# Kernel optimization log

Hardware: AMD Instinct MI355X
Metric: run time of the kernel (lower is better)

## Reference

```python
import jax, jax.numpy as jnp
import numpy as np

D_IN = 1024
D_OUT = 1024
NUM_HEADS = 16
HEAD_DIM = D_OUT // NUM_HEADS


def setup_inputs() -> dict:
    key = jax.random.key(0)
    ks = jax.random.split(key, 6)
    s = 1.0 / np.sqrt(D_IN)
    inputs = jax.random.normal(ks[0], (4, 2048, D_IN), dtype=jnp.float32)
    Wq = jax.random.uniform(ks[1], (D_IN, D_OUT), jnp.float32, -s, s)
    Wk = jax.random.uniform(ks[2], (D_IN, D_OUT), jnp.float32, -s, s)
    Wv = jax.random.uniform(ks[3], (D_IN, D_OUT), jnp.float32, -s, s)
    so = 1.0 / np.sqrt(D_OUT)
    Wo = jax.random.uniform(ks[4], (D_OUT, D_OUT), jnp.float32, -so, so)
    bo = jax.random.uniform(ks[5], (D_OUT,), jnp.float32, -so, so)
    return {"inputs": inputs, "Wq": Wq, "Wk": Wk, "Wv": Wv, "Wo": Wo, "bo": bo}


def reference(inputs, Wq, Wk, Wv, Wo, bo):
    b, n, _ = inputs.shape
    # projections -> [b, h, n, d]
    def split_heads(x):
        return x.reshape(b, n, NUM_HEADS, HEAD_DIM).transpose(0, 2, 1, 3)
    q = split_heads(inputs @ Wq)
    k = split_heads(inputs @ Wk)
    v = split_heads(inputs @ Wv)
    scores = jnp.einsum('bhqd,bhkd->bhqk', q, k) / np.sqrt(HEAD_DIM).astype(np.float32)
    causal = jnp.tril(jnp.ones((n, n), dtype=bool))  # True = keep
    scores = jnp.where(causal, scores, -jnp.inf)
    weights = jax.nn.softmax(scores, axis=-1)
    ctx = jnp.einsum('bhqk,bhkd->bhqd', weights, v)
    ctx = ctx.transpose(0, 2, 1, 3).reshape(b, n, D_OUT)
    return ctx @ Wo + bo
```

## Files before the change

kernel.cpp:

```cpp
#include <hip/hip_runtime.h>

typedef unsigned short u16;
typedef unsigned int u32;
typedef __attribute__((ext_vector_type(8))) short short8;
typedef __attribute__((ext_vector_type(4))) short short4_t;
typedef __attribute__((ext_vector_type(4))) float floatx4;
typedef __attribute__((ext_vector_type(4))) unsigned short ushort4_t;
typedef __attribute__((ext_vector_type(4))) float float4_t;
typedef __attribute__((ext_vector_type(2))) unsigned int uint2_t;


__device__ __forceinline__ u16 f2bf(float f) {
  unsigned u = __builtin_bit_cast(unsigned, f);
  u += 0x7FFFu + ((u >> 16) & 1u);
  return (u16)(u >> 16);
}

__device__ __forceinline__ u32 pack_bf2(float a, float b) {
  u32 ua = __builtin_bit_cast(u32, a) + 0x8000u;
  u32 ub = __builtin_bit_cast(u32, b) + 0x8000u;
  return __builtin_amdgcn_perm(ua, ub, 0x07060302u);
}

__device__ __forceinline__ void gload_lds16(const void* g, void* l) {
  __builtin_amdgcn_global_load_lds(
      (const __attribute__((address_space(1))) void*)g,
      (__attribute__((address_space(3))) void*)l, 16, 0, 0);
}

#define BAR __builtin_amdgcn_s_barrier()
#define LGK0                                              \
  do {                                                    \
    asm volatile("s_waitcnt lgkmcnt(0)" ::: "memory");    \
    __builtin_amdgcn_sched_barrier(0);                    \
  } while (0)
#define VM4 asm volatile("s_waitcnt vmcnt(4)" ::: "memory")
#define VM0 asm volatile("s_waitcnt vmcnt(0)" ::: "memory")


__global__ void cvt_x(const float* __restrict__ src, u16* __restrict__ dst) {
  int i = blockIdx.x * 256 + threadIdx.x;
  float4_t f = ((const float4_t*)src)[i];
  ushort4_t u;
  u.x = f2bf(f.x); u.y = f2bf(f.y); u.z = f2bf(f.z); u.w = f2bf(f.w);
  ((ushort4_t*)dst)[i] = u;
}

__global__ __launch_bounds__(256) void transpose_cvt4(
    const float* __restrict__ wq, const float* __restrict__ wk,
    const float* __restrict__ wv, const float* __restrict__ wo,
    u16* __restrict__ qk, u16* __restrict__ vt, u16* __restrict__ ot, float sc) {
  __shared__ float T[64][65];
  const int which = blockIdx.z;
  const float* s = (which == 0) ? wq : (which == 1) ? wk : (which == 2) ? wv : wo;
  u16* d = (which == 0) ? qk : (which == 1) ? (qk + (1u << 20)) : (which == 2) ? vt : ot;
  const float scale = (which == 0) ? sc : 1.f;
  const int n0 = blockIdx.x * 64, k0 = blockIdx.y * 64;
  const int c = threadIdx.x & 63, rg = threadIdx.x >> 6;
  for (int i = 0; i < 16; ++i) {
    int r = i * 4 + rg;
    T[r][c] = s[(k0 + r) * 1024 + n0 + c];
  }
  __syncthreads();
  for (int i = 0; i < 16; ++i) {
    int r = i * 4 + rg;
    d[(n0 + r) * 1024 + k0 + c] = f2bf(T[c][r] * scale);
  }
}

template <int MODE>
__global__ __launch_bounds__(256) void gemm_bt(
    const u16* __restrict__ A, const u16* __restrict__ Bt, void* __restrict__ Cv,
    const float* __restrict__ bias, int K, int lda, int ldb, int ldc) {
  __shared__ u16 As[2][128 * 32];
  __shared__ u16 Bs[2][128 * 32];
  const int tid = threadIdx.x;
  const int w = tid >> 6, l = tid & 63, quad = l >> 4, l16 = l & 15;
  const int wm = w >> 1, wn = w & 1;
  const size_t m0 = (size_t)blockIdx.y * 128, n0 = (size_t)blockIdx.x * 128;

  floatx4 acc[4][4];
  for (int i = 0; i < 4; ++i)
    for (int j = 0; j < 4; ++j) acc[i][j] = (floatx4){0.f, 0.f, 0.f, 0.f};

  auto stage = [&](int k0, int buf) {
    for (int i = 0; i < 2; ++i) {
      int c = i * 256 + tid;
      int row = c >> 2, off = (c & 3) * 8;
      gload_lds16(A + (m0 + row) * (size_t)lda + k0 + off, &As[buf][c * 8]);
      gload_lds16(Bt + (n0 + row) * (size_t)ldb + k0 + off, &Bs[buf][c * 8]);
    }
  };

  const int nk = K >> 5;
  stage(0, 0);
  __syncthreads();

  for (int ki = 0; ki < nk; ++ki) {
    const int buf = ki & 1;
    if (ki + 1 < nk) stage((ki + 1) << 5, buf ^ 1);

    short8 a[4], bb[4];
    for (int im = 0; im < 4; ++im)
      a[im] = *(const short8*)&As[buf][(wm * 64 + im * 16 + l16) * 32 + quad * 8];
    for (int in = 0; in < 4; ++in)
      bb[in] = *(const short8*)&Bs[buf][(wn * 64 + in * 16 + l16) * 32 + quad * 8];
    for (int im = 0; im < 4; ++im)
      for (int in = 0; in < 4; ++in)
        acc[im][in] = __builtin_amdgcn_mfma_f32_16x16x32_bf16(a[im], bb[in], acc[im][in], 0, 0, 0);

    __syncthreads();
  }

  for (int im = 0; im < 4; ++im)
    for (int in = 0; in < 4; ++in) {
      size_t r0 = m0 + wm * 64 + im * 16 + quad * 4;
      size_t col = n0 + wn * 64 + in * 16 + l16;
      float bv = (MODE == 1) ? bias[col] : 0.f;
      for (int r = 0; r < 4; ++r) {
        float val = acc[im][in][r] + bv;
        if (MODE == 0)
          ((u16*)Cv)[(r0 + r) * (size_t)ldc + col] = f2bf(val);
        else
          ((float*)Cv)[(r0 + r) * (size_t)ldc + col] = val;
      }
    }
}

__global__ __launch_bounds__(512, 2) void gemm256_bt(
    const u16* __restrict__ A, const u16* __restrict__ Bt, u16* __restrict__ C,
    int K, int lda, int ldb, int ldc) {
  __shared__ u16 As[2][256 * 64];
  __shared__ u16 Bs[2][256 * 64];
  const int tid = threadIdx.x;
  const int l = tid & 63, quad = l >> 4, l16 = l & 15;
  const int w = tid >> 6, wm = w >> 2, wn = w & 3;

  const int orig = blockIdx.x + 8 * blockIdx.y;
  const int tsw = (orig & 7) * 32 + (orig >> 3);
  const size_t m0 = (size_t)(tsw >> 3) * 256, n0 = (size_t)(tsw & 7) * 256;
  const int NT = K >> 6;

  floatx4 acc[8][4];
#pragma unroll
  for (int i = 0; i < 8; ++i)
#pragma unroll
    for (int j = 0; j < 4; ++j) acc[i][j] = (floatx4){0.f, 0.f, 0.f, 0.f};

  auto stage = [&](int isB, int t, int h) {
    const u16* src = isB ? Bt : A;
    const size_t rb = isB ? n0 : m0;
    const int ld = isB ? ldb : lda;
    u16* lds = (isB ? &Bs[t & 1][0] : &As[t & 1][0]) + h * 8192;
    const int k0 = t << 6;
#pragma unroll
    for (int r = 0; r < 2; ++r) {
      int idx = r * 512 + tid;
      int rr = idx >> 3;
      int ce = ((idx & 7) ^ (rr & 7)) << 3;
      gload_lds16(src + (rb + h * 128 + rr) * (size_t)ld + k0 + ce, lds + idx * 8);
    }
  };

  const int swz = (l16 & 7) << 4;
  const int ca0 = (quad * 16) ^ swz;
  const int ca1 = (64 + quad * 16) ^ swz;
  const char* aB = (const char*)&As[0][0];
  const char* bB = (const char*)&Bs[0][0];
  const int arow = (wm * 128 + l16) * 128;
  const int brow = (wn * 64 + l16) * 128;

  short8 a[4][2], b[2][2][2];

  auto readA = [&](int buf, int mh) {
#pragma unroll
    for (int ii = 0; ii < 4; ++ii) {
      const char* p = aB + buf * 32768 + arow + mh * 8192 + ii * 2048;
      a[ii][0] = *(const short8*)(p + ca0);
      a[ii][1] = *(const short8*)(p + ca1);
    }
  };
  auto readB = [&](int buf, int nh) {
#pragma unroll
    for (int jj = 0; jj < 2; ++jj) {
      const char* p = bB + buf * 32768 + brow + nh * 4096 + jj * 2048;
      b[nh][jj][0] = *(const short8*)(p + ca0);
      b[nh][jj][1] = *(const short8*)(p + ca1);
    }
  };
  auto mmaq = [&](int mh, int nh) {
    __builtin_amdgcn_s_setprio(1);
#pragma unroll
    for (int ii = 0; ii < 4; ++ii)
#pragma unroll
      for (int jj = 0; jj < 2; ++jj) {
        acc[mh * 4 + ii][nh * 2 + jj] = __builtin_amdgcn_mfma_f32_16x16x32_bf16(
            a[ii][0], b[nh][jj][0], acc[mh * 4 + ii][nh * 2 + jj], 0, 0, 0);
        acc[mh * 4 + ii][nh * 2 + jj] = __builtin_amdgcn_mfma_f32_16x16x32_bf16(
            a[ii][1], b[nh][jj][1], acc[mh * 4 + ii][nh * 2 + jj], 0, 0, 0);
      }
    __builtin_amdgcn_s_setprio(0);
  };

  stage(1, 0, 0); stage(1, 0, 1); stage(0, 0, 0); stage(0, 0, 1);
  stage(1, 1, 0); stage(1, 1, 1);
  VM4;
  BAR;

  const int nit = NT >> 1;
  for (int i = 0; i < nit; ++i) {
    const int t0 = 2 * i;
    const bool last = (i + 1 == nit);
    readA(0, 0); readB(0, 0);
    stage(0, t0 + 1, 0);
    BAR; LGK0; mmaq(0, 0); BAR;
    readB(0, 1);
    stage(0, t0 + 1, 1);
    BAR; LGK0; mmaq(0, 1); BAR;
    readA(0, 1);
    if (t0 + 2 < NT) stage(1, t0 + 2, 0);
    BAR; LGK0; mmaq(1, 1); BAR;
    if (t0 + 2 < NT) stage(1, t0 + 2, 1);
    mmaq(1, 0);
    if (last) { VM0; } else { VM4; }
    BAR;
    readA(1, 0); readB(1, 0);
    if (t0 + 2 < NT) stage(0, t0 + 2, 0);
    BAR; LGK0; mmaq(0, 0); BAR;
    readB(1, 1);
    if (t0 + 2 < NT) stage(0, t0 + 2, 1);
    BAR; LGK0; mmaq(0, 1); BAR;
    readA(1, 1);
    if (t0 + 3 < NT) stage(1, t0 + 3, 0);
    BAR; LGK0; mmaq(1, 1); BAR;
    if (t0 + 3 < NT) stage(1, t0 + 3, 1);
    mmaq(1, 0);
    VM4; BAR;
  }

#pragma unroll
  for (int iF = 0; iF < 8; ++iF)
#pragma unroll
    for (int jF = 0; jF < 4; ++jF) {
      size_t r0 = m0 + wm * 128 + iF * 16 + quad * 4;
      size_t col = n0 + wn * 64 + jF * 16 + l16;
#pragma unroll
      for (int r = 0; r < 4; ++r)
        C[(r0 + r) * (size_t)ldc + col] = f2bf(acc[iF][jF][r]);
    }
}

__global__ __launch_bounds__(256, 2) void flash_attn(
    const u16* __restrict__ QK, const u16* __restrict__ Vt, u16* __restrict__ ctx) {
  __shared__ u16 Ks[2][64 * 64];
  __shared__ u16 Vs[2][64 * 64];

  const int tid = threadIdx.x;
  const int w = tid >> 6, l = tid & 63, quad = l >> 4, l16 = l & 15;
  const int bh = blockIdx.x, p = blockIdx.y;
  const int b = bh >> 4, h = bh & 15;
  const int xr = (l16 & 7) << 4;

  const int qtA = 15 - p, qtB = p;
  const int nktA = 2 * qtA + 2, ntot = nktA + 2 * qtB + 2;

  auto stage = [&](int kt, int buf) {
    for (int i = 0; i < 2; ++i) {
      int c = i * 256 + tid;
      int row = c >> 3, scol = ((c & 7) ^ (row & 7)) << 3;
      gload_lds16(QK + (size_t)(b * 2048 + kt * 64 + row) * 2048 + 1024 + h * 64 + scol,
                  &Ks[buf][c * 8]);
      gload_lds16(Vt + (size_t)(h * 64 + row) * 8192 + b * 2048 + kt * 64 + scol,
                  &Vs[buf][c * 8]);
    }
  };

  short8 aq[2][2];
  floatx4 o[2][4];
  float lsum[2];

  auto load_q = [&](int q0w) {
    for (int qf = 0; qf < 2; ++qf) {
      const size_t base = (size_t)(b * 2048 + q0w + qf * 16 + l16) * 2048 + h * 64 + quad * 8;
      aq[qf][0] = *(const short8*)(QK + base);
      aq[qf][1] = *(const short8*)(QK + base + 32);
    }
    for (int qf = 0; qf < 2; ++qf) {
      lsum[qf] = 0.f;
      for (int df = 0; df < 4; ++df) o[qf][df] = (floatx4){0.f, 0.f, 0.f, 0.f};
    }
  };

  auto epilogue = [&](int q0w) {
    for (int qf = 0; qf < 2; ++qf) {
      float t = lsum[qf];
      t += __shfl_xor(t, 16, 64);
      t += __shfl_xor(t, 32, 64);
      float inv = __builtin_amdgcn_rcpf(t);
      size_t row = (size_t)(b * 2048 + q0w + qf * 16 + l16);
      for (int df = 0; df < 4; ++df) {
        ushort4_t st;
        for (int r = 0; r < 4; ++r) st[r] = f2bf(o[qf][df][r] * inv);
        *(ushort4_t*)(ctx + row * 1024 + h * 64 + df * 16 + quad * 4) = st;
      }
    }
  };

  int q0w = qtA * 128 + w * 32;
  int ktmax_w = (q0w + 31) >> 6;
  load_q(q0w);
  stage(0, 0);
  __syncthreads();

  for (int t = 0; t < ntot; ++t) {
    const int buf = t & 1;
    const int kt = (t < nktA) ? t : t - nktA;
    if (t + 1 < ntot) {
      int tn = t + 1;
      stage((tn < nktA) ? tn : tn - nktA, buf ^ 1);
    }

    if (kt <= ktmax_w) {
      const bool need_mask = (kt == ktmax_w);

      short8 ka[4][2];
      for (int nf = 0; nf < 4; ++nf) {
        const char* kb = (const char*)&Ks[buf][0] + (nf * 16 + l16) * 128;
        ka[nf][0] = *(const short8*)(kb + ((quad * 16) ^ xr));
        ka[nf][1] = *(const short8*)(kb + ((64 + quad * 16) ^ xr));
      }
      short4_t va[4][4];
      for (int df = 0; df < 4; ++df) {
        const char* vb = (const char*)&Vs[buf][0] + (df * 16 + l16) * 128;
        for (int nf = 0; nf < 4; ++nf)
          va[nf][df] = *(const short4_t*)(vb + ((nf * 32 + quad * 8) ^ xr));
      }

      for (int qf = 0; qf < 2; ++qf) {
        floatx4 s[4];
        for (int nf = 0; nf < 4; ++nf) s[nf] = (floatx4){0.f, 0.f, 0.f, 0.f};
        __builtin_amdgcn_s_setprio(1);
        for (int nf = 0; nf < 4; ++nf) {
          s[nf] = __builtin_amdgcn_mfma_f32_16x16x32_bf16(ka[nf][0], aq[qf][0], s[nf], 0, 0, 0);
          s[nf] = __builtin_amdgcn_mfma_f32_16x16x32_bf16(ka[nf][1], aq[qf][1], s[nf], 0, 0, 0);
        }
        __builtin_amdgcn_s_setprio(0);
        if (need_mask) {
          int qpos = q0w + qf * 16 + l16;
          for (int nf = 0; nf < 4; ++nf)
            for (int r = 0; r < 4; ++r) {
              int kpos = kt * 64 + nf * 16 + quad * 4 + r;
              if (kpos > qpos) s[nf][r] = -1e30f;
            }
        }
        for (int nf = 0; nf < 4; ++nf) {
          float p0 = __builtin_amdgcn_exp2f(s[nf][0]);
          float p1 = __builtin_amdgcn_exp2f(s[nf][1]);
          float p2 = __builtin_amdgcn_exp2f(s[nf][2]);
          float p3 = __builtin_amdgcn_exp2f(s[nf][3]);
          lsum[qf] += (p0 + p1) + (p2 + p3);
          uint2_t pk;
          pk.x = pack_bf2(p1, p0);
          pk.y = pack_bf2(p3, p2);
          short4_t pb = __builtin_bit_cast(short4_t, pk);
          __builtin_amdgcn_s_setprio(1);
          for (int df = 0; df < 4; ++df)
            o[qf][df] = __builtin_amdgcn_mfma_f32_16x16x16bf16_1k(va[nf][df], pb, o[qf][df], 0, 0, 0);
          __builtin_amdgcn_s_setprio(0);
        }
      }
    }
    __syncthreads();

    if (t == nktA - 1) {
      epilogue(q0w);
      q0w = qtB * 128 + w * 32;
      ktmax_w = (q0w + 31) >> 6;
      load_q(q0w);
    }
  }
  epilogue(q0w);
}


extern "C" void kernel_launch(void* const* d_in, const int* in_sizes, int n_in,
                              void* d_out, int out_size, void* d_ws, size_t ws_size,
                              hipStream_t stream) {
  const float* X  = (const float*)d_in[0];
  const float* Wq = (const float*)d_in[1];
  const float* Wk = (const float*)d_in[2];
  const float* Wv = (const float*)d_in[3];
  const float* Wo = (const float*)d_in[4];
  const float* bo = (const float*)d_in[5];

  char* ws = (char*)d_ws;
  u16* Xb   = (u16*)(ws);
  u16* WqkT = (u16*)(ws + (16u << 20));
  u16* WvT  = (u16*)(ws + (20u << 20));
  u16* WoT  = (u16*)(ws + (22u << 20));
  u16* QKb  = (u16*)(ws + (24u << 20));
  u16* Vt   = (u16*)(ws + (56u << 20));

  const float SC = 0.125f * 1.44269504088896340736f;

  cvt_x<<<8192, 256, 0, stream>>>(X, Xb);
  transpose_cvt4<<<dim3(16, 16, 4), 256, 0, stream>>>(Wq, Wk, Wv, Wo, WqkT, WvT, WoT, SC);

  gemm256_bt<<<dim3(8, 32), 512, 0, stream>>>(Xb, WqkT, QKb, 1024, 1024, 1024, 2048);
  gemm_bt<0><<<dim3(64, 8), 256, 0, stream>>>(WvT, Xb, Vt, nullptr, 1024, 1024, 1024, 8192);

  flash_attn<<<dim3(64, 8), 256, 0, stream>>>(QKb, Vt, Xb);

  gemm_bt<1><<<dim3(8, 64), 256, 0, stream>>>(Xb, WoT, (float*)d_out, bo, 1024, 1024, 1024, 1024);
}
```

Baseline: 253.0 us.

## Split flash attention into 8 waves of 16 query rows each

The flash attention block grows from 4 to 8 waves, and each wave now owns 16 query rows instead of 32. This halves per-wave accumulator and Q register state and lets one load instruction per thread stage each K/V tile. V fragments are now loaded per key fragment, not all up front. The probability pack is replaced with the hardware v_cvt_pk_bf16_f32 instruction, which rounds differently from the previous +0x8000 truncation. Each K/V tile is now reused by fewer rows per wave, so LDS reads per MFMA roughly double.

Result: faster. 243.5 us (-3.7%).

```diff
diff --git a/kernel.cpp b/kernel.cpp
--- a/kernel.cpp
+++ b/kernel.cpp
@@ -16,10 +16,10 @@
   return (u16)(u >> 16);
 }
 
-__device__ __forceinline__ u32 pack_bf2(float a, float b) {
-  u32 ua = __builtin_bit_cast(u32, a) + 0x8000u;
-  u32 ub = __builtin_bit_cast(u32, b) + 0x8000u;
-  return __builtin_amdgcn_perm(ua, ub, 0x07060302u);
+__device__ __forceinline__ u32 cvt_pk_bf16(float a, float b) {
+  u32 r;
+  asm("v_cvt_pk_bf16_f32 %0, %1, %2" : "=v"(r) : "v"(a), "v"(b));
+  return r;
 }
 
 __device__ __forceinline__ void gload_lds16(const void* g, void* l) {
@@ -250,7 +250,7 @@
     }
 }
 
-__global__ __launch_bounds__(256, 2) void flash_attn(
+__global__ __launch_bounds__(512, 4) void flash_attn(
     const u16* __restrict__ QK, const u16* __restrict__ Vt, u16* __restrict__ ctx) {
   __shared__ u16 Ks[2][64 * 64];
   __shared__ u16 Vs[2][64 * 64];
@@ -265,49 +265,41 @@
   const int nktA = 2 * qtA + 2, ntot = nktA + 2 * qtB + 2;
 
   auto stage = [&](int kt, int buf) {
-    for (int i = 0; i < 2; ++i) {
-      int c = i * 256 + tid;
-      int row = c >> 3, scol = ((c & 7) ^ (row & 7)) << 3;
-      gload_lds16(QK + (size_t)(b * 2048 + kt * 64 + row) * 2048 + 1024 + h * 64 + scol,
-                  &Ks[buf][c * 8]);
-      gload_lds16(Vt + (size_t)(h * 64 + row) * 8192 + b * 2048 + kt * 64 + scol,
-                  &Vs[buf][c * 8]);
-    }
-  };
-
-  short8 aq[2][2];
-  floatx4 o[2][4];
-  float lsum[2];
+    int c = tid;
+    int row = c >> 3, scol = ((c & 7) ^ (row & 7)) << 3;
+    gload_lds16(QK + (size_t)(b * 2048 + kt * 64 + row) * 2048 + 1024 + h * 64 + scol,
+                &Ks[buf][c * 8]);
+    gload_lds16(Vt + (size_t)(h * 64 + row) * 8192 + b * 2048 + kt * 64 + scol,
+                &Vs[buf][c * 8]);
+  };
+
+  short8 aq[2];
+  floatx4 o[4];
+  float lsum;
 
   auto load_q = [&](int q0w) {
-    for (int qf = 0; qf < 2; ++qf) {
-      const size_t base = (size_t)(b * 2048 + q0w + qf * 16 + l16) * 2048 + h * 64 + quad * 8;
-      aq[qf][0] = *(const short8*)(QK + base);
-      aq[qf][1] = *(const short8*)(QK + base + 32);
-    }
-    for (int qf = 0; qf < 2; ++qf) {
-      lsum[qf] = 0.f;
-      for (int df = 0; df < 4; ++df) o[qf][df] = (floatx4){0.f, 0.f, 0.f, 0.f};
-    }
+    const size_t base = (size_t)(b * 2048 + q0w + l16) * 2048 + h * 64 + quad * 8;
+    aq[0] = *(const short8*)(QK + base);
+    aq[1] = *(const short8*)(QK + base + 32);
+    lsum = 0.f;
+    for (int df = 0; df < 4; ++df) o[df] = (floatx4){0.f, 0.f, 0.f, 0.f};
   };
 
   auto epilogue = [&](int q0w) {
-    for (int qf = 0; qf < 2; ++qf) {
-      float t = lsum[qf];
-      t += __shfl_xor(t, 16, 64);
-      t += __shfl_xor(t, 32, 64);
-      float inv = __builtin_amdgcn_rcpf(t);
-      size_t row = (size_t)(b * 2048 + q0w + qf * 16 + l16);
-      for (int df = 0; df < 4; ++df) {
-        ushort4_t st;
-        for (int r = 0; r < 4; ++r) st[r] = f2bf(o[qf][df][r] * inv);
-        *(ushort4_t*)(ctx + row * 1024 + h * 64 + df * 16 + quad * 4) = st;
-      }
-    }
-  };
-
-  int q0w = qtA * 128 + w * 32;
-  int ktmax_w = (q0w + 31) >> 6;
+    float t = lsum;
+    t += __shfl_xor(t, 16, 64);
+    t += __shfl_xor(t, 32, 64);
+    float inv = __builtin_amdgcn_rcpf(t);
+    size_t row = (size_t)(b * 2048 + q0w + l16);
+    for (int df = 0; df < 4; ++df) {
+      ushort4_t st;
+      for (int r = 0; r < 4; ++r) st[r] = f2bf(o[df][r] * inv);
+      *(ushort4_t*)(ctx + row * 1024 + h * 64 + df * 16 + quad * 4) = st;
+    }
+  };
+
+  int q0w = qtA * 128 + w * 16;
+  int ktmax_w = (q0w + 15) >> 6;
   load_q(q0w);
   stage(0, 0);
   __syncthreads();
@@ -329,53 +321,50 @@
         ka[nf][0] = *(const short8*)(kb + ((quad * 16) ^ xr));
         ka[nf][1] = *(const short8*)(kb + ((64 + quad * 16) ^ xr));
       }
-      short4_t va[4][4];
-      for (int df = 0; df < 4; ++df) {
-        const char* vb = (const char*)&Vs[buf][0] + (df * 16 + l16) * 128;
+
+      floatx4 s[4];
+      for (int nf = 0; nf < 4; ++nf) s[nf] = (floatx4){0.f, 0.f, 0.f, 0.f};
+      __builtin_amdgcn_s_setprio(1);
+      for (int nf = 0; nf < 4; ++nf) {
+        s[nf] = __builtin_amdgcn_mfma_f32_16x16x32_bf16(ka[nf][0], aq[0], s[nf], 0, 0, 0);
+        s[nf] = __builtin_amdgcn_mfma_f32_16x16x32_bf16(ka[nf][1], aq[1], s[nf], 0, 0, 0);
+      }
+      __builtin_amdgcn_s_setprio(0);
+      if (need_mask) {
+        int qpos = q0w + l16;
         for (int nf = 0; nf < 4; ++nf)
-          va[nf][df] = *(const short4_t*)(vb + ((nf * 32 + quad * 8) ^ xr));
-      }
-
-      for (int qf = 0; qf < 2; ++qf) {
-        floatx4 s[4];
-        for (int nf = 0; nf < 4; ++nf) s[nf] = (floatx4){0.f, 0.f, 0.f, 0.f};
+          for (int r = 0; r < 4; ++r) {
+            int kpos = kt * 64 + nf * 16 + quad * 4 + r;
+            if (kpos > qpos) s[nf][r] = -1e30f;
+          }
+      }
+      for (int nf = 0; nf < 4; ++nf) {
+        short4_t va[4];
+        for (int df = 0; df < 4; ++df) {
+          const char* vb = (const char*)&Vs[buf][0] + (df * 16 + l16) * 128;
+          va[df] = *(const short4_t*)(vb + ((nf * 32 + quad * 8) ^ xr));
+        }
+        float p0 = __builtin_amdgcn_exp2f(s[nf][0]);
+        float p1 = __builtin_amdgcn_exp2f(s[nf][1]);
+        float p2 = __builtin_amdgcn_exp2f(s[nf][2]);
+        float p3 = __builtin_amdgcn_exp2f(s[nf][3]);
+        lsum += (p0 + p1) + (p2 + p3);
+        uint2_t pk;
+        pk.x = cvt_pk_bf16(p0, p1);
+        pk.y = cvt_pk_bf16(p2, p3);
+        short4_t pb = __builtin_bit_cast(short4_t, pk);
         __builtin_amdgcn_s_setprio(1);
-        for (int nf = 0; nf < 4; ++nf) {
-          s[nf] = __builtin_amdgcn_mfma_f32_16x16x32_bf16(ka[nf][0], aq[qf][0], s[nf], 0, 0, 0);
-          s[nf] = __builtin_amdgcn_mfma_f32_16x16x32_bf16(ka[nf][1], aq[qf][1], s[nf], 0, 0, 0);
-        }
+        for (int df = 0; df < 4; ++df)
+          o[df] = __builtin_amdgcn_mfma_f32_16x16x16bf16_1k(va[df], pb, o[df], 0, 0, 0);
         __builtin_amdgcn_s_setprio(0);
-        if (need_mask) {
-          int qpos = q0w + qf * 16 + l16;
-          for (int nf = 0; nf < 4; ++nf)
-            for (int r = 0; r < 4; ++r) {
-              int kpos = kt * 64 + nf * 16 + quad * 4 + r;
-              if (kpos > qpos) s[nf][r] = -1e30f;
-            }
-        }
-        for (int nf = 0; nf < 4; ++nf) {
-          float p0 = __builtin_amdgcn_exp2f(s[nf][0]);
-          float p1 = __builtin_amdgcn_exp2f(s[nf][1]);
-          float p2 = __builtin_amdgcn_exp2f(s[nf][2]);
-          float p3 = __builtin_amdgcn_exp2f(s[nf][3]);
-          lsum[qf] += (p0 + p1) + (p2 + p3);
-          uint2_t pk;
-          pk.x = pack_bf2(p1, p0);
-          pk.y = pack_bf2(p3, p2);
-          short4_t pb = __builtin_bit_cast(short4_t, pk);
-          __builtin_amdgcn_s_setprio(1);
-          for (int df = 0; df < 4; ++df)
-            o[qf][df] = __builtin_amdgcn_mfma_f32_16x16x16bf16_1k(va[nf][df], pb, o[qf][df], 0, 0, 0);
-          __builtin_amdgcn_s_setprio(0);
-        }
       }
     }
     __syncthreads();
 
     if (t == nktA - 1) {
       epilogue(q0w);
-      q0w = qtB * 128 + w * 32;
-      ktmax_w = (q0w + 31) >> 6;
+      q0w = qtB * 128 + w * 16;
+      ktmax_w = (q0w + 15) >> 6;
       load_q(q0w);
     }
   }
@@ -409,7 +398,7 @@
   gemm256_bt<<<dim3(8, 32), 512, 0, stream>>>(Xb, WqkT, QKb, 1024, 1024, 1024, 2048);
   gemm_bt<0><<<dim3(64, 8), 256, 0, stream>>>(WvT, Xb, Vt, nullptr, 1024, 1024, 1024, 8192);
 
-  flash_attn<<<dim3(64, 8), 256, 0, stream>>>(QKb, Vt, Xb);
+  flash_attn<<<dim3(64, 8), 512, 0, stream>>>(QKb, Vt, Xb);
 
   gemm_bt<1><<<dim3(8, 64), 256, 0, stream>>>(Xb, WoT, (float*)d_out, bo, 1024, 1024, 1024, 1024);
 }
```
